# Kernel optimization log

Measured on AMD Instinct MI355X. Metric: run time of the kernel, lower is better.

## Reference

```python
import jax, jax.numpy as jnp
import numpy as np

MAX_X = 128
B, S, H, D = 2, 512, 8, 64
E = H * D  # embed_dim = 512


def setup_inputs() -> dict:
    key = jax.random.key(0)
    k1, k2, k3 = jax.random.split(key, 3)
    q = jax.random.normal(k1, (B, S, H, D), dtype=jnp.float32)
    embed_table = jax.random.normal(k2, (2 * MAX_X + 1, E), dtype=jnp.float32)
    x = jax.random.randint(k3, (B, S), 0, MAX_X, dtype=jnp.int64)
    return {"q": q, "embed_table": embed_table, "x": x, "max_x": MAX_X}


def reference(q, embed_table, x, max_x):
    # rel[b, i, j] = max_x + x[b, j] - x[b, i]  (faithful to x.reshape(-1,1,S) - x.reshape(-1,S,1))
    rel = max_x + x[:, None, :] - x[:, :, None]          # [B, S, S] int
    rel_e = embed_table[rel]                              # [B, S, S, E] gather
    b, s = rel.shape[0], rel.shape[1]
    h, d = q.shape[2], q.shape[3]
    rel_e = rel_e.reshape(b, s, s, h, d)                  # [B, Sq, Sk, H, D]
    # scores[b, h, q, k] = sum_d q[b, q, h, d] * rel_e[b, q, k, h, d]
    return jnp.einsum('bqhd,bqkhd->bhqk', q, rel_e)
```

## Files before the change

### kernel.cpp

```cpp
#include <hip/hip_runtime.h>


#define S_LEN 512
#define NH 8
#define HD 64
#define EDIM 512
#define TI 16
#define NR 256
#define TPAD 72
#define OPAD 257

typedef __attribute__((ext_vector_type(8))) short bf16x8;
typedef __attribute__((ext_vector_type(4))) float f32x4;

__device__ __forceinline__ unsigned short f2bf(float f) {
    union { float f; unsigned u; } v; v.f = f;
    unsigned r = v.u + 0x7fffu + ((v.u >> 16) & 1u);
    return (unsigned short)(r >> 16);
}

__global__ __launch_bounds__(256) void relpos_kernel(
    const float* __restrict__ q,
    const float* __restrict__ et,
    const int*   __restrict__ x,
    const int*   __restrict__ maxx_p,
    float*       __restrict__ out)
{
    const int tid = threadIdx.x;
    const int per = S_LEN / TI;
    const int b   = blockIdx.x / (NH * per);
    const int h   = (blockIdx.x / per) % NH;
    const int i0  = (blockIdx.x % per) * TI;

    __shared__ unsigned short Tl[NR][TPAD];
    __shared__ unsigned short Ql[TI][TPAD];
    __shared__ float          Ts[TI][OPAD];
    __shared__ int            xi_s[TI];

    const int row16 = tid >> 4;
    const int k4    = tid & 15;

    #pragma unroll
    for (int p = 0; p < 16; ++p) {
        const int r = p * 16 + row16;
        const float4 v = *(const float4*)(et + (size_t)r * EDIM + h * HD + k4 * 4);
        ushort4 u;
        u.x = f2bf(v.x); u.y = f2bf(v.y); u.z = f2bf(v.z); u.w = f2bf(v.w);
        *(ushort4*)&Tl[r][k4 * 4] = u;
    }
    {
        const float4 v = *(const float4*)(q + (((size_t)b * S_LEN + i0 + row16) * NH + h) * HD + k4 * 4);
        ushort4 u;
        u.x = f2bf(v.x); u.y = f2bf(v.y); u.z = f2bf(v.z); u.w = f2bf(v.w);
        *(ushort4*)&Ql[row16][k4 * 4] = u;
    }
    if (tid < TI) xi_s[tid] = x[b * S_LEN + i0 + tid];
    const int2 xj = *(const int2*)(x + b * S_LEN + 2 * tid);
    const int maxx = maxx_p[0];

    __syncthreads();

    const int w    = tid >> 6;
    const int l    = tid & 63;
    const int quad = l >> 4;
    const int c    = l & 15;

    const bf16x8 a0 = *(const bf16x8*)&Ql[c][quad * 8];
    const bf16x8 a1 = *(const bf16x8*)&Ql[c][32 + quad * 8];

    f32x4 acc[4];
    #pragma unroll
    for (int nt = 0; nt < 4; ++nt) acc[nt] = (f32x4){0.f, 0.f, 0.f, 0.f};

    #pragma unroll
    for (int nt = 0; nt < 4; ++nt) {
        const int r = w * 64 + nt * 16 + c;
        const bf16x8 b0 = *(const bf16x8*)&Tl[r][quad * 8];
        const bf16x8 b1 = *(const bf16x8*)&Tl[r][32 + quad * 8];
        acc[nt] = __builtin_amdgcn_mfma_f32_16x16x32_bf16(a0, b0, acc[nt], 0, 0, 0);
        acc[nt] = __builtin_amdgcn_mfma_f32_16x16x32_bf16(a1, b1, acc[nt], 0, 0, 0);
    }

    #pragma unroll
    for (int nt = 0; nt < 4; ++nt) {
        #pragma unroll
        for (int v = 0; v < 4; ++v) {
            Ts[quad * 4 + v][w * 64 + nt * 16 + c] = acc[nt][v];
        }
    }

    __syncthreads();

    float* obase = out + (((size_t)b * NH + h) * S_LEN + i0) * S_LEN;
    #pragma unroll
    for (int ii = 0; ii < TI; ++ii) {
        const int xi = xi_s[ii];
        const int r0 = (maxx + xj.x - xi) & 255;
        const int r1 = (maxx + xj.y - xi) & 255;
        float2 o;
        o.x = Ts[ii][r0];
        o.y = Ts[ii][r1];
        *(float2*)(obase + (size_t)ii * S_LEN + 2 * tid) = o;
    }
}

extern "C" void kernel_launch(void* const* d_in, const int* in_sizes, int n_in,
                              void* d_out, int out_size, void* d_ws, size_t ws_size,
                              hipStream_t stream) {
    const float* q    = (const float*)d_in[0];
    const float* et   = (const float*)d_in[1];
    const int*   x    = (const int*)d_in[2];
    const int*   maxx = (const int*)d_in[3];
    float*       out  = (float*)d_out;

    const int B = in_sizes[2] / S_LEN;
    dim3 grid(B * NH * (S_LEN / TI));
    relpos_kernel<<<grid, 256, 0, stream>>>(q, et, x, maxx, out);
}
```

Before: 67.52 us.

## Precompute bf16 table and q in workspace, load table via direct global-to-LDS

Adds a separate conversion kernel that turns the embedding-table head slices and q into bf16 once, writing the table with an XOR swizzle into workspace. The main kernel then copies its 32KB bf16 table slice into LDS with global_load_lds and reads the q fragments straight from global memory. This replaces the per-block fp32 loads and conversions, which were repeated in each of 512 blocks, and drops the padded LDS layout in favour of a swizzled one. The cost is a second kernel launch and an extra workspace round trip.

New measurement: 69.48 us. 1.03x slower.

```diff
diff --git a/kernel.cpp b/kernel.cpp
--- a/kernel.cpp
+++ b/kernel.cpp
@@ -7,11 +7,14 @@
 #define EDIM 512
 #define TI 16
 #define NR 256
-#define TPAD 72
 #define OPAD 257
 
-typedef __attribute__((ext_vector_type(8))) short bf16x8;
-typedef __attribute__((ext_vector_type(4))) float f32x4;
+#define WS_TBL_ELEMS (NH * NR * HD)
+#define WS_Q_OFF     WS_TBL_ELEMS
+
+typedef __attribute__((ext_vector_type(8))) short    bf16x8;
+typedef __attribute__((ext_vector_type(8))) unsigned short ushort8;
+typedef __attribute__((ext_vector_type(4))) float    f32x4;
 
 __device__ __forceinline__ unsigned short f2bf(float f) {
     union { float f; unsigned u; } v; v.f = f;
@@ -19,9 +22,34 @@
     return (unsigned short)(r >> 16);
 }
 
-__global__ __launch_bounds__(256) void relpos_kernel(
+__global__ __launch_bounds__(256) void cvt_kernel(
     const float* __restrict__ q,
     const float* __restrict__ et,
+    unsigned short* __restrict__ ws)
+{
+    const int t = blockIdx.x * 256 + threadIdx.x;
+    if (blockIdx.x < 64) {
+        const int h  = t >> 11;
+        const int r  = (t >> 3) & 255;
+        const int c8 = t & 7;
+        const float* src = et + (size_t)r * EDIM + h * HD + c8 * 8;
+        const float4 v0 = *(const float4*)src;
+        const float4 v1 = *(const float4*)(src + 4);
+        ushort8 u;
+        u[0] = f2bf(v0.x); u[1] = f2bf(v0.y); u[2] = f2bf(v0.z); u[3] = f2bf(v0.w);
+        u[4] = f2bf(v1.x); u[5] = f2bf(v1.y); u[6] = f2bf(v1.z); u[7] = f2bf(v1.w);
+        *(ushort8*)(ws + ((h * NR + r) * HD) + ((c8 ^ (r & 7)) * 8)) = u;
+    } else {
+        const int idx = (t - 64 * 256) * 4;
+        const float4 v = *(const float4*)(q + idx);
+        ushort4 u;
+        u.x = f2bf(v.x); u.y = f2bf(v.y); u.z = f2bf(v.z); u.w = f2bf(v.w);
+        *(ushort4*)(ws + WS_Q_OFF + idx) = u;
+    }
+}
+
+__global__ __launch_bounds__(256) void relpos_kernel(
+    const unsigned short* __restrict__ ws,
     const int*   __restrict__ x,
     const int*   __restrict__ maxx_p,
     float*       __restrict__ out)
@@ -32,41 +60,35 @@
     const int h   = (blockIdx.x / per) % NH;
     const int i0  = (blockIdx.x % per) * TI;
 
-    __shared__ unsigned short Tl[NR][TPAD];
-    __shared__ unsigned short Ql[TI][TPAD];
+    __shared__ unsigned short Tl[NR * HD];
     __shared__ float          Ts[TI][OPAD];
     __shared__ int            xi_s[TI];
-
-    const int row16 = tid >> 4;
-    const int k4    = tid & 15;
-
-    #pragma unroll
-    for (int p = 0; p < 16; ++p) {
-        const int r = p * 16 + row16;
-        const float4 v = *(const float4*)(et + (size_t)r * EDIM + h * HD + k4 * 4);
-        ushort4 u;
-        u.x = f2bf(v.x); u.y = f2bf(v.y); u.z = f2bf(v.z); u.w = f2bf(v.w);
-        *(ushort4*)&Tl[r][k4 * 4] = u;
-    }
-    {
-        const float4 v = *(const float4*)(q + (((size_t)b * S_LEN + i0 + row16) * NH + h) * HD + k4 * 4);
-        ushort4 u;
-        u.x = f2bf(v.x); u.y = f2bf(v.y); u.z = f2bf(v.z); u.w = f2bf(v.w);
-        *(ushort4*)&Ql[row16][k4 * 4] = u;
-    }
-    if (tid < TI) xi_s[tid] = x[b * S_LEN + i0 + tid];
-    const int2 xj = *(const int2*)(x + b * S_LEN + 2 * tid);
-    const int maxx = maxx_p[0];
-
-    __syncthreads();
 
     const int w    = tid >> 6;
     const int l    = tid & 63;
     const int quad = l >> 4;
     const int c    = l & 15;
 
-    const bf16x8 a0 = *(const bf16x8*)&Ql[c][quad * 8];
-    const bf16x8 a1 = *(const bf16x8*)&Ql[c][32 + quad * 8];
+    const char* gbase = (const char*)(ws + (size_t)h * (NR * HD)) + w * 8192 + l * 16;
+    char* lbase = (char*)Tl + w * 8192;
+    #pragma unroll
+    for (int it = 0; it < 8; ++it) {
+        __builtin_amdgcn_global_load_lds(
+            (const __attribute__((address_space(1))) unsigned int*)(gbase + it * 1024),
+            (__attribute__((address_space(3))) unsigned int*)(lbase + it * 1024),
+            16, 0, 0);
+    }
+
+    const unsigned short* qrow =
+        ws + WS_Q_OFF + (((size_t)(b * S_LEN + i0 + c)) * NH + h) * HD;
+    const bf16x8 a0 = *(const bf16x8*)(qrow + quad * 8);
+    const bf16x8 a1 = *(const bf16x8*)(qrow + 32 + quad * 8);
+
+    if (tid < TI) xi_s[tid] = x[b * S_LEN + i0 + tid];
+    const int2 xj = *(const int2*)(x + b * S_LEN + 2 * tid);
+    const int maxx = maxx_p[0];
+
+    __syncthreads();
 
     f32x4 acc[4];
     #pragma unroll
@@ -74,9 +96,11 @@
 
     #pragma unroll
     for (int nt = 0; nt < 4; ++nt) {
-        const int r = w * 64 + nt * 16 + c;
-        const bf16x8 b0 = *(const bf16x8*)&Tl[r][quad * 8];
-        const bf16x8 b1 = *(const bf16x8*)&Tl[r][32 + quad * 8];
+        const int r  = w * 64 + nt * 16 + c;
+        const int p0 = quad ^ (r & 7);
+        const int p1 = (4 + quad) ^ (r & 7);
+        const bf16x8 b0 = *(const bf16x8*)(Tl + r * HD + p0 * 8);
+        const bf16x8 b1 = *(const bf16x8*)(Tl + r * HD + p1 * 8);
         acc[nt] = __builtin_amdgcn_mfma_f32_16x16x32_bf16(a0, b0, acc[nt], 0, 0, 0);
         acc[nt] = __builtin_amdgcn_mfma_f32_16x16x32_bf16(a1, b1, acc[nt], 0, 0, 0);
     }
@@ -84,9 +108,8 @@
     #pragma unroll
     for (int nt = 0; nt < 4; ++nt) {
         #pragma unroll
-        for (int v = 0; v < 4; ++v) {
+        for (int v = 0; v < 4; ++v)
             Ts[quad * 4 + v][w * 64 + nt * 16 + c] = acc[nt][v];
-        }
     }
 
     __syncthreads();
@@ -112,8 +135,11 @@
     const int*   x    = (const int*)d_in[2];
     const int*   maxx = (const int*)d_in[3];
     float*       out  = (float*)d_out;
+    unsigned short* ws = (unsigned short*)d_ws;
 
     const int B = in_sizes[2] / S_LEN;
-    dim3 grid(B * NH * (S_LEN / TI));
-    relpos_kernel<<<grid, 256, 0, stream>>>(q, et, x, maxx, out);
+
+    cvt_kernel<<<dim3(64 + (B * S_LEN * NH * HD) / 1024), 256, 0, stream>>>(q, et, ws);
+
+    relpos_kernel<<<dim3(B * NH * (S_LEN / TI)), 256, 0, stream>>>(ws, x, maxx, out);
 }
```

## Swizzle LDS table layout, load Q directly to registers, transpose score staging

Applied to the files above, without the earlier changes.

Replaces the padded LDS embedding tile with an XOR-swizzled unpadded layout to avoid bank conflicts, and loads Q straight from global into MFMA A-operand registers, dropping the Q LDS stage. Conversion now uses packed bf16 intrinsics. The score staging buffer is transposed to [row][query] so accumulator writes and gathers use float2 accesses, with a conditional that reuses the paired value when consecutive query rows map to the same relative index. This cuts LDS traffic and conflicts, at the cost of a data-dependent branch in the gather loop.

After: 67.43 us. Within noise of the previous version (-0.1%).

```diff
diff --git a/kernel.cpp b/kernel.cpp
--- a/kernel.cpp
+++ b/kernel.cpp
@@ -1,4 +1,5 @@
 #include <hip/hip_runtime.h>
+#include <hip/hip_bf16.h>
 
 
 #define S_LEN 512
@@ -7,16 +8,15 @@
 #define EDIM 512
 #define TI 16
 #define NR 256
-#define TPAD 72
-#define OPAD 257
+#define TIP 18
 
 typedef __attribute__((ext_vector_type(8))) short bf16x8;
 typedef __attribute__((ext_vector_type(4))) float f32x4;
 
-__device__ __forceinline__ unsigned short f2bf(float f) {
-    union { float f; unsigned u; } v; v.f = f;
-    unsigned r = v.u + 0x7fffu + ((v.u >> 16) & 1u);
-    return (unsigned short)(r >> 16);
+__device__ __forceinline__ ushort2 pk_bf16(float a, float b) {
+    union { __hip_bfloat162 h; ushort2 u; } v;
+    v.h = __float22bfloat162_rn(float2{a, b});
+    return v.u;
 }
 
 __global__ __launch_bounds__(256) void relpos_kernel(
@@ -32,41 +32,46 @@
     const int h   = (blockIdx.x / per) % NH;
     const int i0  = (blockIdx.x % per) * TI;
 
-    __shared__ unsigned short Tl[NR][TPAD];
-    __shared__ unsigned short Ql[TI][TPAD];
-    __shared__ float          Ts[TI][OPAD];
+    __shared__ unsigned short Tl[NR * HD];
+    __shared__ float          Ts[NR][TIP];
     __shared__ int            xi_s[TI];
-
-    const int row16 = tid >> 4;
-    const int k4    = tid & 15;
-
-    #pragma unroll
-    for (int p = 0; p < 16; ++p) {
-        const int r = p * 16 + row16;
-        const float4 v = *(const float4*)(et + (size_t)r * EDIM + h * HD + k4 * 4);
-        ushort4 u;
-        u.x = f2bf(v.x); u.y = f2bf(v.y); u.z = f2bf(v.z); u.w = f2bf(v.w);
-        *(ushort4*)&Tl[r][k4 * 4] = u;
-    }
-    {
-        const float4 v = *(const float4*)(q + (((size_t)b * S_LEN + i0 + row16) * NH + h) * HD + k4 * 4);
-        ushort4 u;
-        u.x = f2bf(v.x); u.y = f2bf(v.y); u.z = f2bf(v.z); u.w = f2bf(v.w);
-        *(ushort4*)&Ql[row16][k4 * 4] = u;
-    }
-    if (tid < TI) xi_s[tid] = x[b * S_LEN + i0 + tid];
-    const int2 xj = *(const int2*)(x + b * S_LEN + 2 * tid);
-    const int maxx = maxx_p[0];
-
-    __syncthreads();
 
     const int w    = tid >> 6;
     const int l    = tid & 63;
     const int quad = l >> 4;
     const int c    = l & 15;
 
-    const bf16x8 a0 = *(const bf16x8*)&Ql[c][quad * 8];
-    const bf16x8 a1 = *(const bf16x8*)&Ql[c][32 + quad * 8];
+    const float* qrow = q + (((size_t)b * S_LEN + i0 + c) * NH + h) * HD;
+    const float4 qa0 = *(const float4*)(qrow + quad * 8);
+    const float4 qa1 = *(const float4*)(qrow + quad * 8 + 4);
+    const float4 qb0 = *(const float4*)(qrow + 32 + quad * 8);
+    const float4 qb1 = *(const float4*)(qrow + 32 + quad * 8 + 4);
+
+    const int rrow = tid >> 4;
+    const int c4   = tid & 15;
+    const int c8   = c4 >> 1;
+    const int half = c4 & 1;
+    #pragma unroll
+    for (int it = 0; it < 16; ++it) {
+        const int r = it * 16 + rrow;
+        const float4 v = *(const float4*)(et + (size_t)r * EDIM + h * HD + c4 * 4);
+        const ushort2 u0 = pk_bf16(v.x, v.y);
+        const ushort2 u1 = pk_bf16(v.z, v.w);
+        ushort4 u; u.x = u0.x; u.y = u0.y; u.z = u1.x; u.w = u1.y;
+        *(ushort4*)(Tl + r * HD + ((c8 ^ (r & 7)) * 8) + half * 4) = u;
+    }
+
+    if (tid < TI) xi_s[tid] = x[b * S_LEN + i0 + tid];
+    const int2 xj = *(const int2*)(x + b * S_LEN + 2 * tid);
+    const int maxx = maxx_p[0];
+
+    union { bf16x8 v; ushort2 u[4]; } a0u, a1u;
+    a0u.u[0] = pk_bf16(qa0.x, qa0.y); a0u.u[1] = pk_bf16(qa0.z, qa0.w);
+    a0u.u[2] = pk_bf16(qa1.x, qa1.y); a0u.u[3] = pk_bf16(qa1.z, qa1.w);
+    a1u.u[0] = pk_bf16(qb0.x, qb0.y); a1u.u[1] = pk_bf16(qb0.z, qb0.w);
+    a1u.u[2] = pk_bf16(qb1.x, qb1.y); a1u.u[3] = pk_bf16(qb1.z, qb1.w);
+
+    __syncthreads();
 
     f32x4 acc[4];
     #pragma unroll
@@ -74,33 +79,40 @@
 
     #pragma unroll
     for (int nt = 0; nt < 4; ++nt) {
-        const int r = w * 64 + nt * 16 + c;
-        const bf16x8 b0 = *(const bf16x8*)&Tl[r][quad * 8];
-        const bf16x8 b1 = *(const bf16x8*)&Tl[r][32 + quad * 8];
-        acc[nt] = __builtin_amdgcn_mfma_f32_16x16x32_bf16(a0, b0, acc[nt], 0, 0, 0);
-        acc[nt] = __builtin_amdgcn_mfma_f32_16x16x32_bf16(a1, b1, acc[nt], 0, 0, 0);
+        const int r  = w * 64 + nt * 16 + c;
+        const int p0 = quad ^ (c & 7);
+        const int p1 = (4 + quad) ^ (c & 7);
+        const bf16x8 b0 = *(const bf16x8*)(Tl + r * HD + p0 * 8);
+        const bf16x8 b1 = *(const bf16x8*)(Tl + r * HD + p1 * 8);
+        acc[nt] = __builtin_amdgcn_mfma_f32_16x16x32_bf16(a0u.v, b0, acc[nt], 0, 0, 0);
+        acc[nt] = __builtin_amdgcn_mfma_f32_16x16x32_bf16(a1u.v, b1, acc[nt], 0, 0, 0);
     }
 
     #pragma unroll
     for (int nt = 0; nt < 4; ++nt) {
-        #pragma unroll
-        for (int v = 0; v < 4; ++v) {
-            Ts[quad * 4 + v][w * 64 + nt * 16 + c] = acc[nt][v];
-        }
+        const int r = w * 64 + nt * 16 + c;
+        *(float2*)&Ts[r][quad * 4]     = float2{acc[nt][0], acc[nt][1]};
+        *(float2*)&Ts[r][quad * 4 + 2] = float2{acc[nt][2], acc[nt][3]};
     }
 
     __syncthreads();
 
     float* obase = out + (((size_t)b * NH + h) * S_LEN + i0) * S_LEN;
     #pragma unroll
-    for (int ii = 0; ii < TI; ++ii) {
-        const int xi = xi_s[ii];
-        const int r0 = (maxx + xj.x - xi) & 255;
-        const int r1 = (maxx + xj.y - xi) & 255;
-        float2 o;
-        o.x = Ts[ii][r0];
-        o.y = Ts[ii][r1];
-        *(float2*)(obase + (size_t)ii * S_LEN + 2 * tid) = o;
+    for (int ii = 0; ii < TI; ii += 2) {
+        const int r0 = (maxx + xj.x - xi_s[ii]) & 255;
+        const int r1 = (maxx + xj.y - xi_s[ii]) & 255;
+        const int r0b = (maxx + xj.x - xi_s[ii + 1]) & 255;
+        const int r1b = (maxx + xj.y - xi_s[ii + 1]) & 255;
+        const float2 g0 = *(const float2*)&Ts[r0][ii];
+        const float2 g1 = *(const float2*)&Ts[r1][ii];
+        float2 o0, o1;
+        o0.x = g0.x;
+        o0.y = g1.x;
+        o1.x = (r0b == r0) ? g0.y : Ts[r0b][ii + 1];
+        o1.y = (r1b == r1) ? g1.y : Ts[r1b][ii + 1];
+        *(float2*)(obase + (size_t)ii * S_LEN + 2 * tid)       = o0;
+        *(float2*)(obase + (size_t)(ii + 1) * S_LEN + 2 * tid) = o1;
     }
 }
 
```
